# Kernel tuning notes

Measured on AMD Instinct MI355X. Metric: run time of the kernel, lower is better.

## Reference

```python
import jax, jax.numpy as jnp
import numpy as np

C_IN, HIDDEN, C_OUT, N_NODE = 200, 128, 2, 200
BATCH = 512

def setup_inputs() -> dict:
    key = jax.random.key(0)
    k1, k2, k3, k4 = jax.random.split(key, 4)
    x = jax.random.normal(k1, (BATCH, N_NODE, C_IN), dtype=jnp.float32)
    adj = jax.random.randint(k2, (BATCH, N_NODE, N_NODE), 0, 2, dtype=jnp.int32)
    # GINConv MLPs (single Linear each); stored as [in, out]
    W1 = jax.random.normal(k3, (C_IN, HIDDEN), dtype=jnp.float32) / np.sqrt(C_IN)
    b1 = jnp.zeros((HIDDEN,), dtype=jnp.float32)
    W2 = jax.random.normal(k4, (HIDDEN, C_OUT), dtype=jnp.float32) / np.sqrt(HIDDEN)
    b2 = jnp.zeros((C_OUT,), dtype=jnp.float32)
    eps1 = jnp.zeros((), dtype=jnp.float32)  # train_eps=True, init 0
    eps2 = jnp.zeros((), dtype=jnp.float32)
    return {"x": x, "adj": adj, "W1": W1, "b1": b1, "W2": W2, "b2": b2, "eps1": eps1, "eps2": eps2}

def _gin_aggregate(adjf, h):
    # edge (b,i,j) sends h[b,i] to node j: agg[b,j] = sum_i adj[b,i,j]*h[b,i]
    return jnp.einsum('bij,bif->bjf', adjf, h)

def reference(x, adj, W1, b1, W2, b2, eps1, eps2):
    adjf = adj.astype(x.dtype)  # binary 0/1 adjacency [B,N,N]
    # GIN layer 1: nn((1+eps)*x + sum_neighbors(x)), then ReLU
    agg1 = _gin_aggregate(adjf, x)
    h = jax.nn.relu(((1.0 + eps1) * x + agg1) @ W1 + b1)
    # GIN layer 2
    agg2 = _gin_aggregate(adjf, h)
    out = ((1.0 + eps2) * h + agg2) @ W2 + b2  # [B,N,2]
    return out.mean(axis=-2)  # [B,2]
```

## Files before the change

### kernel.cpp

```cpp
#include <hip/hip_runtime.h>

#define BATCH 512
#define NNODE 200
#define CIN   200
#define HID   128
#define IPY   232
#define KCH   7

typedef __attribute__((ext_vector_type(4))) float  f32x4;
typedef __attribute__((ext_vector_type(4))) int    i32x4;
typedef __attribute__((ext_vector_type(8))) short  sh8;
typedef __attribute__((ext_vector_type(4))) short  sh4;
typedef __attribute__((ext_vector_type(8))) __bf16 bf16x8;

__device__ __forceinline__ short f2bf(float x) {
  union { float f; unsigned u; } v; v.f = x;
  unsigned r = v.u + 0x7FFFu + ((v.u >> 16) & 1u);
  return (short)(r >> 16);
}
__device__ __forceinline__ f32x4 mfma16(sh8 a, sh8 b, f32x4 c) {
  return __builtin_amdgcn_mfma_f32_16x16x32_bf16(
      __builtin_bit_cast(bf16x8, a), __builtin_bit_cast(bf16x8, b), c, 0, 0, 0);
}
__device__ __forceinline__ f32x4 mfma16i(sh8 a, i32x4 b, f32x4 c) {
  return __builtin_amdgcn_mfma_f32_16x16x32_bf16(
      __builtin_bit_cast(bf16x8, a), __builtin_bit_cast(bf16x8, b), c, 0, 0, 0);
}
__device__ __forceinline__ i32x4 expand8(unsigned byte_) {
  i32x4 w;
#pragma unroll
  for (int h = 0; h < 4; ++h) {
    unsigned p = byte_ >> (2 * h);
    unsigned d = ((p & 1u) ? 0x3F80u : 0u) | ((p & 2u) ? 0x3F800000u : 0u);
    w[h] = (int)d;
  }
  return w;
}

__global__ __launch_bounds__(256) void k_prep(const float* __restrict__ W1,
                                              short* __restrict__ W1T) {
  const int idx = blockIdx.x * 256 + threadIdx.x;
  const int f = idx / IPY, c = idx - f * IPY;
  W1T[idx] = (c < CIN) ? f2bf(W1[(size_t)c * HID + f]) : (short)0;
}

__global__ __launch_bounds__(1024, 4) void k_gin(const float* __restrict__ x,
                                                 const int* __restrict__ adj,
                                                 const short* __restrict__ W1Tg,
                                                 const float* __restrict__ b1,
                                                 const float* __restrict__ W2,
                                                 const float* __restrict__ b2,
                                                 const float* __restrict__ eps1p,
                                                 const float* __restrict__ eps2p,
                                                 float* __restrict__ out) {
  __shared__ __align__(16) short    ls_w1t[HID * IPY];
  __shared__ __align__(16) short    ls_y  [HID * IPY];
  __shared__ __align__(16) unsigned ls_bits[KCH * 224];
  __shared__ __align__(16) float    ls_deg[224];
  __shared__               float    ls_part[13][2];

  const int b    = blockIdx.x;
  const int tid  = threadIdx.x;
  const int wave = tid >> 6, lane = tid & 63;
  const int lq   = lane >> 4, lm = lane & 15;
  const int* adjb = adj + (size_t)b * NNODE * NNODE;

  sh8 af[KCH];

  if (wave >= 13) {
    const int iw  = wave - 13;
    const int wd0 = iw * 2, wd1 = (iw == 2) ? 7 : iw * 2 + 2;
    const int jc3 = min(192 + lane, NNODE - 1);
    for (int wd = wd0; wd < wd1; ++wd) {
      const int tmax = (wd == 6) ? 8 : 32;
      unsigned w0 = 0, w1 = 0, w2 = 0, w3 = 0;
      for (int t8 = 0; t8 < tmax; t8 += 8) {
        int v0[8], v1[8], v2[8], v3[8];
#pragma unroll
        for (int rr = 0; rr < 8; ++rr) {
          const int* rp = adjb + (wd * 32 + t8 + rr) * NNODE;
          v0[rr] = rp[lane]; v1[rr] = rp[64 + lane];
          v2[rr] = rp[128 + lane]; v3[rr] = rp[jc3];
        }
#pragma unroll
        for (int rr = 0; rr < 8; ++rr) {
          const int t = t8 + rr;
          const unsigned b0 = (unsigned)v0[rr] & 1u;
          const unsigned b1_ = (unsigned)v1[rr] & 1u;
          const unsigned b2_ = (unsigned)v2[rr] & 1u;
          const unsigned b3_ = (lane < 8) ? ((unsigned)v3[rr] & 1u) : 0u;
          w0 |= b0 << t; w1 |= b1_ << t; w2 |= b2_ << t; w3 |= b3_ << t;
          const int dg = __popcll(__ballot(b0 != 0u)) + __popcll(__ballot(b1_ != 0u))
                       + __popcll(__ballot(b2_ != 0u)) + __popcll(__ballot(b3_ != 0u));
          if (lane == 0) ls_deg[wd * 32 + t] = (float)dg;
        }
      }
      unsigned* bp = &ls_bits[wd * 224];
      bp[lane] = w0; bp[64 + lane] = w1; bp[128 + lane] = w2;
      if (lane < 32) bp[192 + lane] = w3;
    }
  } else {
    sh8 sc[5];
    int chs[5];
#pragma unroll
    for (int it = 0; it < 5; ++it) {
      chs[it] = wave + it * 13;
      if (chs[it] < 58) sc[it] = ((const sh8*)W1Tg)[chs[it] * 64 + lane];
    }
    f32x4 px0[KCH], px1[KCH];
    const int row = min(wave * 16 + lm, NNODE - 1);
    const float* xr = x + (size_t)b * NNODE * CIN + (size_t)row * CIN;
#pragma unroll
    for (int k = 0; k < KCH; ++k) {
      const int c0 = k * 32 + lq * 8;
      f32x4 z = {0.f, 0.f, 0.f, 0.f};
      px0[k] = z; px1[k] = z;
      if (c0 < CIN) { px0[k] = *(const f32x4*)(xr + c0); px1[k] = *(const f32x4*)(xr + c0 + 4); }
    }
#pragma unroll
    for (int it = 0; it < 5; ++it)
      if (chs[it] < 58) ((sh8*)ls_w1t)[chs[it] * 64 + lane] = sc[it];
    if (tid < 384) {
      const int f = tid / 3, p = tid - f * 3;
      sh8 z = {0, 0, 0, 0, 0, 0, 0, 0};
      *(sh8*)&ls_y[f * IPY + 200 + p * 8] = z;
    }
#pragma unroll
    for (int k = 0; k < KCH; ++k) {
      sh8 a;
#pragma unroll
      for (int jj = 0; jj < 4; ++jj) { a[jj] = f2bf(px0[k][jj]); a[4 + jj] = f2bf(px1[k][jj]); }
      af[k] = a;
    }
  }
  __syncthreads();

  if (wave < 13) {
    const int mt = wave;
#pragma unroll 2
    for (int ft = 0; ft < 8; ++ft) {
      const int fb = ft * 16;
      const short* wr = &ls_w1t[(fb + lm) * IPY];
      f32x4 acc = {0.f, 0.f, 0.f, 0.f};
#pragma unroll
      for (int k = 0; k < KCH; ++k)
        acc = mfma16(af[k], *(const sh8*)(wr + k * 32 + lq * 8), acc);
      sh4 st;
#pragma unroll
      for (int r = 0; r < 4; ++r) st[r] = f2bf(acc[r]);
      if (mt * 16 + lq * 4 < NNODE)
        *(sh4*)&ls_y[(fb + lm) * IPY + mt * 16 + lq * 4] = st;
    }
  }
  __syncthreads();

  if (wave < 13) {
    const float e1 = eps1p[0], e2 = eps2p[0];
    const int jt = wave;
    const int j  = jt * 16 + lm;
    const bool jok = (j < NNODE);
    const unsigned cd0 = (unsigned)(unsigned short)f2bf(1.f + e1);
    const unsigned cd1 = (unsigned)(unsigned short)f2bf(2.f + e1);
    unsigned bwa[KCH];
#pragma unroll
    for (int k = 0; k < KCH; ++k) bwa[k] = ls_bits[k * 224 + j];
    i32x4 bfr[KCH];
#pragma unroll
    for (int k = 0; k < KCH; ++k) {
      const unsigned byte_ = (bwa[k] >> (lq * 8)) & 0xFFu;
      i32x4 w = expand8(byte_);
      const int d = j - (k * 32 + lq * 8);
      if (d >= 0 && d < 8) {
        const unsigned val = ((byte_ >> d) & 1u) ? cd1 : cd0;
        const int h2 = d >> 1, sh = (d & 1) * 16;
        w[h2] = (int)(((unsigned)w[h2] & ~(0xFFFFu << sh)) | (val << sh));
      }
      bfr[k] = w;
    }
    float ga = 0.f, gb = 0.f;
#pragma unroll 2
    for (int ft = 0; ft < 8; ++ft) {
      const int fb = ft * 16;
      const short* yr = &ls_y[(fb + lm) * IPY];
      f32x4 acc = {0.f, 0.f, 0.f, 0.f};
#pragma unroll
      for (int k = 0; k < KCH; ++k)
        acc = mfma16i(*(const sh8*)(yr + k * 32 + lq * 8), bfr[k], acc);
      const f32x4 b1v = *(const f32x4*)(b1 + fb + lq * 4);
      const f32x4 w2a = *(const f32x4*)(W2 + (fb + lq * 4) * 2);
      const f32x4 w2b = *(const f32x4*)(W2 + (fb + lq * 4) * 2 + 4);
#pragma unroll
      for (int r = 0; r < 4; ++r) {
        const float h = fmaxf(acc[r] + b1v[r], 0.f);
        const float wc0 = (r == 0) ? w2a[0] : (r == 1) ? w2a[2] : (r == 2) ? w2b[0] : w2b[2];
        const float wc1 = (r == 0) ? w2a[1] : (r == 1) ? w2a[3] : (r == 2) ? w2b[1] : w2b[3];
        ga += h * wc0;
        gb += h * wc1;
      }
    }
    ga += __shfl_xor(ga, 16); ga += __shfl_xor(ga, 32);
    gb += __shfl_xor(gb, 16); gb += __shfl_xor(gb, 32);
    const float wj = 1.f + e2 + ls_deg[min(j, NNODE - 1)];
    float t0 = jok ? wj * ga : 0.f;
    float t1 = jok ? wj * gb : 0.f;
#pragma unroll
    for (int d = 1; d < 16; d <<= 1) { t0 += __shfl_xor(t0, d); t1 += __shfl_xor(t1, d); }
    if (lane == 0) { ls_part[jt][0] = t0; ls_part[jt][1] = t1; }
  }
  __syncthreads();

  if (tid < 2) {
    float s = 0.f;
#pragma unroll
    for (int q = 0; q < 13; ++q) s += ls_part[q][tid];
    out[b * 2 + tid] = b2[tid] + s * (1.f / NNODE);
  }
}

extern "C" void kernel_launch(void* const* d_in, const int* in_sizes, int n_in,
                              void* d_out, int out_size, void* d_ws, size_t ws_size,
                              hipStream_t stream) {
  const float* x    = (const float*)d_in[0];
  const int*   adj  = (const int*)d_in[1];
  const float* W1   = (const float*)d_in[2];
  const float* b1   = (const float*)d_in[3];
  const float* W2   = (const float*)d_in[4];
  const float* b2   = (const float*)d_in[5];
  const float* eps1 = (const float*)d_in[6];
  const float* eps2 = (const float*)d_in[7];
  float* out = (float*)d_out;

  short* W1T = (short*)d_ws;

  k_prep<<<116, 256, 0, stream>>>(W1, W1T);
  k_gin <<<BATCH, 1024, 0, stream>>>(x, adj, W1T, b1, W2, b2, eps1, eps2, out);
}
```

Measured before the change: 211.0 us.

## Stream Y through a 16-row LDS slab per feature tile instead of full buffer

Replaces the full HID×IPY bf16 LDS buffer for the projected features with a 16-row slab, interleaving the W1 projection and the adjacency aggregation per 16-feature tile with barriers between them. The self term (1+eps1) is now added from the slab instead of being folded into the diagonal of the adjacency fragment. b1 and W2 are staged into LDS, and the launch-bounds occupancy hint rises from 4 to 8. This cuts LDS use per block, which may allow more resident blocks, but adds 16 block-wide barriers and serialises the two matmul phases per tile.

```diff
diff --git a/kernel.cpp b/kernel.cpp
--- a/kernel.cpp
+++ b/kernel.cpp
@@ -18,6 +18,10 @@
   unsigned r = v.u + 0x7FFFu + ((v.u >> 16) & 1u);
   return (short)(r >> 16);
 }
+__device__ __forceinline__ float bf2f(short s) {
+  union { unsigned u; float f; } v; v.u = ((unsigned)(unsigned short)s) << 16;
+  return v.f;
+}
 __device__ __forceinline__ f32x4 mfma16(sh8 a, sh8 b, f32x4 c) {
   return __builtin_amdgcn_mfma_f32_16x16x32_bf16(
       __builtin_bit_cast(bf16x8, a), __builtin_bit_cast(bf16x8, b), c, 0, 0, 0);
@@ -44,7 +48,7 @@
   W1T[idx] = (c < CIN) ? f2bf(W1[(size_t)c * HID + f]) : (short)0;
 }
 
-__global__ __launch_bounds__(1024, 4) void k_gin(const float* __restrict__ x,
+__global__ __launch_bounds__(1024, 8) void k_gin(const float* __restrict__ x,
                                                  const int* __restrict__ adj,
                                                  const short* __restrict__ W1Tg,
                                                  const float* __restrict__ b1,
@@ -54,9 +58,10 @@
                                                  const float* __restrict__ eps2p,
                                                  float* __restrict__ out) {
   __shared__ __align__(16) short    ls_w1t[HID * IPY];
-  __shared__ __align__(16) short    ls_y  [HID * IPY];
+  __shared__ __align__(16) short    ls_slab[16 * IPY];
   __shared__ __align__(16) unsigned ls_bits[KCH * 224];
   __shared__ __align__(16) float    ls_deg[224];
+  __shared__ __align__(16) float    ls_w2b1[384];
   __shared__               float    ls_part[13][2];
 
   const int b    = blockIdx.x;
@@ -117,14 +122,17 @@
       px0[k] = z; px1[k] = z;
       if (c0 < CIN) { px0[k] = *(const f32x4*)(xr + c0); px1[k] = *(const f32x4*)(xr + c0 + 4); }
     }
+    float wv = 0.f;
+    if (tid < 384) wv = (tid < 128) ? b1[tid] : W2[tid - 128];
 #pragma unroll
     for (int it = 0; it < 5; ++it)
       if (chs[it] < 58) ((sh8*)ls_w1t)[chs[it] * 64 + lane] = sc[it];
-    if (tid < 384) {
-      const int f = tid / 3, p = tid - f * 3;
+    if (tid < 64) {
+      const int rw = tid >> 2, p = tid & 3;
       sh8 z = {0, 0, 0, 0, 0, 0, 0, 0};
-      *(sh8*)&ls_y[f * IPY + 200 + p * 8] = z;
-    }
+      *(sh8*)&ls_slab[rw * IPY + 200 + p * 8] = z;
+    }
+    if (tid < 384) ls_w2b1[tid] = wv;
 #pragma unroll
     for (int k = 0; k < KCH; ++k) {
       sh8 a;
@@ -135,11 +143,18 @@
   }
   __syncthreads();
 
+  const float e1 = eps1p[0], e2 = eps2p[0];
+  const int j = wave * 16 + lm;
+  unsigned by[KCH];
   if (wave < 13) {
-    const int mt = wave;
-#pragma unroll 2
-    for (int ft = 0; ft < 8; ++ft) {
-      const int fb = ft * 16;
+#pragma unroll
+    for (int k = 0; k < KCH; ++k) by[k] = (ls_bits[k * 224 + j] >> (lq * 8)) & 0xFFu;
+  }
+  float ga = 0.f, gb = 0.f;
+
+  for (int ft = 0; ft < 8; ++ft) {
+    const int fb = ft * 16;
+    if (wave < 13) {
       const short* wr = &ls_w1t[(fb + lm) * IPY];
       f32x4 acc = {0.f, 0.f, 0.f, 0.f};
 #pragma unroll
@@ -148,64 +163,37 @@
       sh4 st;
 #pragma unroll
       for (int r = 0; r < 4; ++r) st[r] = f2bf(acc[r]);
-      if (mt * 16 + lq * 4 < NNODE)
-        *(sh4*)&ls_y[(fb + lm) * IPY + mt * 16 + lq * 4] = st;
-    }
-  }
-  __syncthreads();
+      *(sh4*)&ls_slab[lm * IPY + wave * 16 + lq * 4] = st;
+    }
+    __syncthreads();
+    if (wave < 13) {
+      const short* yr = &ls_slab[lm * IPY];
+      f32x4 accP = {0.f, 0.f, 0.f, 0.f};
+#pragma unroll
+      for (int k = 0; k < KCH; ++k)
+        accP = mfma16i(*(const sh8*)(yr + k * 32 + lq * 8), expand8(by[k]), accP);
+#pragma unroll
+      for (int r = 0; r < 4; ++r) {
+        const int f = fb + lq * 4 + r;
+        const float yself = bf2f(ls_slab[(lq * 4 + r) * IPY + j]);
+        const float h = fmaxf(accP[r] + (1.f + e1) * yself + ls_w2b1[f], 0.f);
+        ga += h * ls_w2b1[128 + 2 * f];
+        gb += h * ls_w2b1[129 + 2 * f];
+      }
+    }
+    __syncthreads();
+  }
 
   if (wave < 13) {
-    const float e1 = eps1p[0], e2 = eps2p[0];
-    const int jt = wave;
-    const int j  = jt * 16 + lm;
-    const bool jok = (j < NNODE);
-    const unsigned cd0 = (unsigned)(unsigned short)f2bf(1.f + e1);
-    const unsigned cd1 = (unsigned)(unsigned short)f2bf(2.f + e1);
-    unsigned bwa[KCH];
-#pragma unroll
-    for (int k = 0; k < KCH; ++k) bwa[k] = ls_bits[k * 224 + j];
-    i32x4 bfr[KCH];
-#pragma unroll
-    for (int k = 0; k < KCH; ++k) {
-      const unsigned byte_ = (bwa[k] >> (lq * 8)) & 0xFFu;
-      i32x4 w = expand8(byte_);
-      const int d = j - (k * 32 + lq * 8);
-      if (d >= 0 && d < 8) {
-        const unsigned val = ((byte_ >> d) & 1u) ? cd1 : cd0;
-        const int h2 = d >> 1, sh = (d & 1) * 16;
-        w[h2] = (int)(((unsigned)w[h2] & ~(0xFFFFu << sh)) | (val << sh));
-      }
-      bfr[k] = w;
-    }
-    float ga = 0.f, gb = 0.f;
-#pragma unroll 2
-    for (int ft = 0; ft < 8; ++ft) {
-      const int fb = ft * 16;
-      const short* yr = &ls_y[(fb + lm) * IPY];
-      f32x4 acc = {0.f, 0.f, 0.f, 0.f};
-#pragma unroll
-      for (int k = 0; k < KCH; ++k)
-        acc = mfma16i(*(const sh8*)(yr + k * 32 + lq * 8), bfr[k], acc);
-      const f32x4 b1v = *(const f32x4*)(b1 + fb + lq * 4);
-      const f32x4 w2a = *(const f32x4*)(W2 + (fb + lq * 4) * 2);
-      const f32x4 w2b = *(const f32x4*)(W2 + (fb + lq * 4) * 2 + 4);
-#pragma unroll
-      for (int r = 0; r < 4; ++r) {
-        const float h = fmaxf(acc[r] + b1v[r], 0.f);
-        const float wc0 = (r == 0) ? w2a[0] : (r == 1) ? w2a[2] : (r == 2) ? w2b[0] : w2b[2];
-        const float wc1 = (r == 0) ? w2a[1] : (r == 1) ? w2a[3] : (r == 2) ? w2b[1] : w2b[3];
-        ga += h * wc0;
-        gb += h * wc1;
-      }
-    }
     ga += __shfl_xor(ga, 16); ga += __shfl_xor(ga, 32);
     gb += __shfl_xor(gb, 16); gb += __shfl_xor(gb, 32);
+    const bool jok = (j < NNODE);
     const float wj = 1.f + e2 + ls_deg[min(j, NNODE - 1)];
     float t0 = jok ? wj * ga : 0.f;
     float t1 = jok ? wj * gb : 0.f;
 #pragma unroll
     for (int d = 1; d < 16; d <<= 1) { t0 += __shfl_xor(t0, d); t1 += __shfl_xor(t1, d); }
-    if (lane == 0) { ls_part[jt][0] = t0; ls_part[jt][1] = t1; }
+    if (lane == 0) { ls_part[wave][0] = t0; ls_part[wave][1] = t1; }
   }
   __syncthreads();
 
```

Result: slower. 252.1 us (+19.5%).
